# Kernel tuning notes

Hardware: AMD Instinct MI355X
Metric: run time of the kernel (lower is better)

Reference implementation:

```python
import jax, jax.numpy as jnp
import numpy as np

NUM_CLASSES = 19
EPSILON = 1e-05


def setup_inputs() -> dict:
    key = jax.random.key(0)
    k1, k2 = jax.random.split(key)
    shape = (16, 1024, 1024)
    y_pred = jax.random.randint(k1, shape, 0, NUM_CLASSES, dtype=jnp.int64 if jax.config.read('jax_enable_x64') else jnp.int32)
    y = jax.random.randint(k2, shape, 0, NUM_CLASSES, dtype=y_pred.dtype)
    return {"y_pred": y_pred, "y": y}


def reference(y_pred, y):
    # Flatten label maps; compute all per-class counts in one pass via bincount
    yp = y_pred.reshape(-1)
    yt = y.reshape(-1)
    # count of (y == i)
    count_y = jnp.bincount(yt, length=NUM_CLASSES).astype(jnp.float32)
    # count of (y_pred == i)
    count_p = jnp.bincount(yp, length=NUM_CLASSES).astype(jnp.float32)
    # intersection_i = count(y == i AND y_pred == i): histogram of y where labels agree
    agree = (yp == yt).astype(jnp.float32)
    inter = jnp.bincount(yt, weights=agree, length=NUM_CLASSES)
    # union_i = |A| + |B| - |A & B|
    union = count_y + count_p - inter
    dice_coeffs = (2.0 * inter + EPSILON) / (union + EPSILON)
    dice_loss = 1.0 - jnp.mean(dice_coeffs)
    return dice_loss
```

## Files before the change

### kernel.cpp

```cpp
#include <hip/hip_runtime.h>

#define NC 19
#define NB 361
#define NCPY 32
#define EPS 1e-5f
#define BS 256
#define GRID 2048

typedef int v4i __attribute__((ext_vector_type(4)));

__global__ __launch_bounds__(BS, 4) void joint_hist_kernel(
    const v4i* __restrict__ yp, const v4i* __restrict__ yt,
    unsigned int* __restrict__ gJ, int n4)
{
    __shared__ unsigned int sJ[4 * NB];
    const int tid = threadIdx.x;
    unsigned int* mine = &sJ[(tid >> 6) * NB];

    for (int i = tid; i < 4 * NB; i += BS) sJ[i] = 0u;
    __syncthreads();

    const int nth = gridDim.x * BS;
    int i = blockIdx.x * BS + tid;

    for (; i + 7 * nth < n4; i += 8 * nth) {
        v4i p[8], t[8];
        #pragma unroll
        for (int u = 0; u < 8; ++u) {
            p[u] = __builtin_nontemporal_load(&yp[i + u * nth]);
            t[u] = __builtin_nontemporal_load(&yt[i + u * nth]);
        }
        #pragma unroll
        for (int u = 0; u < 8; ++u) {
            atomicAdd(&mine[t[u].x * NC + p[u].x], 1u);
            atomicAdd(&mine[t[u].y * NC + p[u].y], 1u);
            atomicAdd(&mine[t[u].z * NC + p[u].z], 1u);
            atomicAdd(&mine[t[u].w * NC + p[u].w], 1u);
        }
    }
    for (; i < n4; i += nth) {
        v4i p = __builtin_nontemporal_load(&yp[i]);
        v4i t = __builtin_nontemporal_load(&yt[i]);
        atomicAdd(&mine[t.x * NC + p.x], 1u);
        atomicAdd(&mine[t.y * NC + p.y], 1u);
        atomicAdd(&mine[t.z * NC + p.z], 1u);
        atomicAdd(&mine[t.w * NC + p.w], 1u);
    }
    __syncthreads();

    unsigned int* myg = &gJ[(blockIdx.x & (NCPY - 1)) * NB];
    for (int b = tid; b < NB; b += BS) {
        unsigned int v = sJ[b] + sJ[NB + b] + sJ[2 * NB + b] + sJ[3 * NB + b];
        if (v) atomicAdd(&myg[b], v);
    }
}

__global__ __launch_bounds__(512) void dice_final_kernel(
    const unsigned int* __restrict__ gJ, float* __restrict__ out)
{
    __shared__ unsigned int J[NB];
    const int tid = threadIdx.x;

    if (tid < NB) {
        unsigned int s = 0;
        #pragma unroll
        for (int c = 0; c < NCPY; ++c) s += gJ[c * NB + tid];
        J[tid] = s;
    }
    __syncthreads();

    if (tid < 64) {
        float dice = 0.0f;
        if (tid < NC) {
            float inter = (float)J[tid * NC + tid];
            float cy = 0.0f, cp = 0.0f;
            #pragma unroll
            for (int j = 0; j < NC; ++j) {
                cy += (float)J[tid * NC + j];
                cp += (float)J[j * NC + tid];
            }
            float uni = cy + cp - inter;
            dice = (2.0f * inter + EPS) / (uni + EPS);
        }
        #pragma unroll
        for (int off = 32; off > 0; off >>= 1)
            dice += __shfl_down(dice, off, 64);
        if (tid == 0) out[0] = 1.0f - dice / (float)NC;
    }
}

extern "C" void kernel_launch(void* const* d_in, const int* in_sizes, int n_in,
                              void* d_out, int out_size, void* d_ws, size_t ws_size,
                              hipStream_t stream)
{
    const v4i* yp = (const v4i*)d_in[0];
    const v4i* yt = (const v4i*)d_in[1];
    unsigned int* gJ = (unsigned int*)d_ws;
    float* out = (float*)d_out;

    const int n = in_sizes[0];
    const int n4 = n >> 2;

    hipMemsetAsync(d_ws, 0, NCPY * NB * sizeof(unsigned int), stream);

    joint_hist_kernel<<<GRID, BS, 0, stream>>>(yp, yt, gJ, n4);
    dice_final_kernel<<<1, 512, 0, stream>>>(gJ, out);
}
```

Measured before the change: 142.8 us.

## Replace LDS joint histogram with packed register counters and DPP wave reductions

Drops the 19x19 joint histogram built with LDS atomics. Each thread instead keeps three marginal counts (true, predicted, agreement) in packed 3-bit fields of 64-bit registers, splits them into even and odd 6-bit lanes, and reduces across the wave with DPP adds. Each thread handles exactly 32 elements and the grid is sized to cover the input, removing the grid-stride loop. This removes heavy LDS atomic contention, but it depends on tight field-width limits (at most 7 per 3-bit field per step, and 16-bit wave sums) holding for this per-thread count, and out-of-range padding uses class 19 (shift 57) so it stays out of the counted classes.

Measured after the change: 146.1 us. 2.3% more time.

```diff
diff --git a/kernel.cpp b/kernel.cpp
--- a/kernel.cpp
+++ b/kernel.cpp
@@ -1,92 +1,132 @@
 #include <hip/hip_runtime.h>
 
 #define NC 19
-#define NB 361
 #define NCPY 32
+#define CSLOT 64
 #define EPS 1e-5f
 #define BS 256
-#define GRID 2048
+#define KPT 8
 
 typedef int v4i __attribute__((ext_vector_type(4)));
 
-__global__ __launch_bounds__(BS, 4) void joint_hist_kernel(
+#define ME 0x01C71C71C71C71C7ULL
+
+__device__ __forceinline__ unsigned wave_sum_dpp(unsigned v) {
+    v += (unsigned)__builtin_amdgcn_update_dpp(0, (int)v, 0x111, 0xF, 0xF, true);
+    v += (unsigned)__builtin_amdgcn_update_dpp(0, (int)v, 0x112, 0xF, 0xF, true);
+    v += (unsigned)__builtin_amdgcn_update_dpp(0, (int)v, 0x114, 0xF, 0xF, true);
+    v += (unsigned)__builtin_amdgcn_update_dpp(0, (int)v, 0x118, 0xF, 0xF, true);
+    v += (unsigned)__builtin_amdgcn_update_dpp(0, (int)v, 0x142, 0xA, 0xF, true);
+    v += (unsigned)__builtin_amdgcn_update_dpp(0, (int)v, 0x143, 0xC, 0xF, true);
+    return v;
+}
+
+__global__ __launch_bounds__(BS) void count_kernel(
     const v4i* __restrict__ yp, const v4i* __restrict__ yt,
     unsigned int* __restrict__ gJ, int n4)
 {
-    __shared__ unsigned int sJ[4 * NB];
     const int tid = threadIdx.x;
-    unsigned int* mine = &sJ[(tid >> 6) * NB];
+    const int nth = (int)gridDim.x * BS;
+    const int base = (int)blockIdx.x * BS + tid;
 
-    for (int i = tid; i < 4 * NB; i += BS) sJ[i] = 0u;
-    __syncthreads();
-
-    const int nth = gridDim.x * BS;
-    int i = blockIdx.x * BS + tid;
-
-    for (; i + 7 * nth < n4; i += 8 * nth) {
-        v4i p[8], t[8];
-        #pragma unroll
-        for (int u = 0; u < 8; ++u) {
-            p[u] = __builtin_nontemporal_load(&yp[i + u * nth]);
-            t[u] = __builtin_nontemporal_load(&yt[i + u * nth]);
-        }
-        #pragma unroll
-        for (int u = 0; u < 8; ++u) {
-            atomicAdd(&mine[t[u].x * NC + p[u].x], 1u);
-            atomicAdd(&mine[t[u].y * NC + p[u].y], 1u);
-            atomicAdd(&mine[t[u].z * NC + p[u].z], 1u);
-            atomicAdd(&mine[t[u].w * NC + p[u].w], 1u);
+    v4i P[KPT], T[KPT];
+    #pragma unroll
+    for (int u = 0; u < KPT; ++u) {
+        const int idx = base + u * nth;
+        if (idx < n4) {
+            P[u] = __builtin_nontemporal_load(&yp[idx]);
+            T[u] = __builtin_nontemporal_load(&yt[idx]);
+        } else {
+            P[u] = (v4i){NC, NC, NC, NC};
+            T[u] = (v4i){NC, NC, NC, NC};
         }
     }
-    for (; i < n4; i += nth) {
-        v4i p = __builtin_nontemporal_load(&yp[i]);
-        v4i t = __builtin_nontemporal_load(&yt[i]);
-        atomicAdd(&mine[t.x * NC + p.x], 1u);
-        atomicAdd(&mine[t.y * NC + p.y], 1u);
-        atomicAdd(&mine[t.z * NC + p.z], 1u);
-        atomicAdd(&mine[t.w * NC + p.w], 1u);
+
+    unsigned long long St = 0, Sp = 0, Si = 0;
+    unsigned long long SEt = 0, SOt = 0, SEp = 0, SOp = 0,
+                       SEi = 0, SOi = 0;
+
+#define UPD(tt, pp) {                                              \
+        const int t_ = (tt), p_ = (pp);                            \
+        const unsigned long long ot = 1ULL << (3 * t_);            \
+        St += ot;                                                  \
+        Sp += 1ULL << (3 * p_);                                    \
+        if (t_ == p_) Si += ot;                                    \
+    }
+
+    #pragma unroll
+    for (int u = 0; u < KPT; ++u) {
+        UPD(T[u].x, P[u].x)
+        UPD(T[u].y, P[u].y)
+        UPD(T[u].z, P[u].z)
+        UPD(T[u].w, P[u].w)
+        SEt += St & ME; SOt += (St >> 3) & ME; St = 0;
+        SEp += Sp & ME; SOp += (Sp >> 3) & ME; Sp = 0;
+        SEi += Si & ME; SOi += (Si >> 3) & ME; Si = 0;
+    }
+#undef UPD
+
+    unsigned pk[30];
+#define PACK(SE, SO, off) {                                        \
+        _Pragma("unroll")                                          \
+        for (int j = 0; j < 10; ++j) {                             \
+            unsigned lo = (unsigned)(((SE) >> (6 * j)) & 63ULL);   \
+            unsigned hi = (j < 9) ? (unsigned)(((SO) >> (6 * j)) & 63ULL) : 0u; \
+            pk[(off) + j] = lo | (hi << 16);                       \
+        }                                                          \
+    }
+    PACK(SEt, SOt, 0)
+    PACK(SEp, SOp, 10)
+    PACK(SEi, SOi, 20)
+#undef PACK
+
+    #pragma unroll
+    for (int j = 0; j < 30; ++j) pk[j] = wave_sum_dpp(pk[j]);
+
+    __shared__ unsigned sW[BS / 64][32];
+    const int wave = tid >> 6, lane = tid & 63;
+    if (lane == 63) {
+        #pragma unroll
+        for (int j = 0; j < 30; ++j) sW[wave][j] = pk[j];
     }
     __syncthreads();
 
-    unsigned int* myg = &gJ[(blockIdx.x & (NCPY - 1)) * NB];
-    for (int b = tid; b < NB; b += BS) {
-        unsigned int v = sJ[b] + sJ[NB + b] + sJ[2 * NB + b] + sJ[3 * NB + b];
-        if (v) atomicAdd(&myg[b], v);
+    if (tid < 57) {
+        const int h = tid / NC, c = tid % NC;
+        const int sh = (c & 1) << 4, j = c >> 1;
+        unsigned v = 0;
+        #pragma unroll
+        for (int w = 0; w < BS / 64; ++w)
+            v += (sW[w][h * 10 + j] >> sh) & 0xFFFFu;
+        atomicAdd(&gJ[(blockIdx.x & (NCPY - 1)) * CSLOT + tid], v);
     }
 }
 
-__global__ __launch_bounds__(512) void dice_final_kernel(
+__global__ __launch_bounds__(64) void dice_final_kernel(
     const unsigned int* __restrict__ gJ, float* __restrict__ out)
 {
-    __shared__ unsigned int J[NB];
     const int tid = threadIdx.x;
-
-    if (tid < NB) {
-        unsigned int s = 0;
+    __shared__ unsigned cnt[57];
+    if (tid < 57) {
+        unsigned s = 0;
         #pragma unroll
-        for (int c = 0; c < NCPY; ++c) s += gJ[c * NB + tid];
-        J[tid] = s;
+        for (int c = 0; c < NCPY; ++c) s += gJ[c * CSLOT + tid];
+        cnt[tid] = s;
     }
     __syncthreads();
 
-    if (tid < 64) {
-        float dice = 0.0f;
-        if (tid < NC) {
-            float inter = (float)J[tid * NC + tid];
-            float cy = 0.0f, cp = 0.0f;
-            #pragma unroll
-            for (int j = 0; j < NC; ++j) {
-                cy += (float)J[tid * NC + j];
-                cp += (float)J[j * NC + tid];
-            }
-            float uni = cy + cp - inter;
-            dice = (2.0f * inter + EPS) / (uni + EPS);
-        }
-        #pragma unroll
-        for (int off = 32; off > 0; off >>= 1)
-            dice += __shfl_down(dice, off, 64);
-        if (tid == 0) out[0] = 1.0f - dice / (float)NC;
+    float dice = 0.0f;
+    if (tid < NC) {
+        float ct = (float)cnt[tid];
+        float cp = (float)cnt[NC + tid];
+        float ci = (float)cnt[2 * NC + tid];
+        float uni = ct + cp - ci;
+        dice = (2.0f * ci + EPS) / (uni + EPS);
     }
+    #pragma unroll
+    for (int off = 32; off > 0; off >>= 1)
+        dice += __shfl_down(dice, off, 64);
+    if (tid == 0) out[0] = 1.0f - dice / (float)NC;
 }
 
 extern "C" void kernel_launch(void* const* d_in, const int* in_sizes, int n_in,
@@ -101,8 +141,10 @@
     const int n = in_sizes[0];
     const int n4 = n >> 2;
 
-    hipMemsetAsync(d_ws, 0, NCPY * NB * sizeof(unsigned int), stream);
+    hipMemsetAsync(d_ws, 0, NCPY * CSLOT * sizeof(unsigned int), stream);
 
-    joint_hist_kernel<<<GRID, BS, 0, stream>>>(yp, yt, gJ, n4);
-    dice_final_kernel<<<1, 512, 0, stream>>>(gJ, out);
+    const int grid = (n4 + BS * KPT - 1) / (BS * KPT);
+
+    count_kernel<<<grid, BS, 0, stream>>>(yp, yt, gJ, n4);
+    dice_final_kernel<<<1, 64, 0, stream>>>(gJ, out);
 }
```

## Replace unrolled batch loads with atomic-add-zero software prefetch ahead of stream

Applied to the files above, without the earlier changes.

Halves the grid and replaces the 8-deep unrolled register batching with a simple grid-stride loop. One lane in eight issues atomicAdd(…, 0) on the input lines PFD strides ahead, pulling those lines toward L2 before they are loaded. This writes through atomics into the read-only input buffers, which adds atomic traffic and can contend with the loads. Dropping the unroll also cuts memory-level parallelism per thread, so latency hiding now rests on the prefetch.

Result: no change. 143.5 us (+0.5%).

```diff
diff --git a/kernel.cpp b/kernel.cpp
--- a/kernel.cpp
+++ b/kernel.cpp
@@ -5,7 +5,8 @@
 #define NCPY 32
 #define EPS 1e-5f
 #define BS 256
-#define GRID 2048
+#define GRID 1024
+#define PFD 2
 
 typedef int v4i __attribute__((ext_vector_type(4)));
 
@@ -20,27 +21,31 @@
     for (int i = tid; i < 4 * NB; i += BS) sJ[i] = 0u;
     __syncthreads();
 
-    const int nth = gridDim.x * BS;
-    int i = blockIdx.x * BS + tid;
+    const int nth = (int)gridDim.x * BS;
+    const bool pf_lane = (tid & 7) == 0;
+    unsigned int* up = (unsigned int*)yp;
+    unsigned int* ut = (unsigned int*)yt;
 
-    for (; i + 7 * nth < n4; i += 8 * nth) {
-        v4i p[8], t[8];
+    if (pf_lane) {
         #pragma unroll
-        for (int u = 0; u < 8; ++u) {
-            p[u] = __builtin_nontemporal_load(&yp[i + u * nth]);
-            t[u] = __builtin_nontemporal_load(&yt[i + u * nth]);
-        }
-        #pragma unroll
-        for (int u = 0; u < 8; ++u) {
-            atomicAdd(&mine[t[u].x * NC + p[u].x], 1u);
-            atomicAdd(&mine[t[u].y * NC + p[u].y], 1u);
-            atomicAdd(&mine[t[u].z * NC + p[u].z], 1u);
-            atomicAdd(&mine[t[u].w * NC + p[u].w], 1u);
+        for (int d = 0; d < PFD; ++d) {
+            const int j = (int)blockIdx.x * BS + tid + d * nth;
+            if (j < n4) {
+                atomicAdd(&up[4 * j], 0u);
+                atomicAdd(&ut[4 * j], 0u);
+            }
         }
     }
-    for (; i < n4; i += nth) {
-        v4i p = __builtin_nontemporal_load(&yp[i]);
-        v4i t = __builtin_nontemporal_load(&yt[i]);
+
+    for (int i = (int)blockIdx.x * BS + tid; i < n4; i += nth) {
+        const v4i p = __builtin_nontemporal_load(&yp[i]);
+        const v4i t = __builtin_nontemporal_load(&yt[i]);
+        __builtin_amdgcn_sched_barrier(0);
+        const int j = i + PFD * nth;
+        if (pf_lane && j < n4) {
+            atomicAdd(&up[4 * j], 0u);
+            atomicAdd(&ut[4 * j], 0u);
+        }
         atomicAdd(&mine[t.x * NC + p.x], 1u);
         atomicAdd(&mine[t.y * NC + p.y], 1u);
         atomicAdd(&mine[t.z * NC + p.z], 1u);
```
